# Optimization experiments

Hardware: AMD Instinct MI355X
Metric: run time of the kernel (lower is better)

## Reference

```python
import jax, jax.numpy as jnp
import numpy as np

B, S, D = 8, 4096, 1024  # batch, seq, input_dim == hidden_dim


def setup_inputs() -> dict:
    key = jax.random.key(0)
    k1, k2, k3, k4, k5 = jax.random.split(key, 5)
    s = 1.0 / np.sqrt(D)
    return {
        "q": jax.random.normal(k1, (B, S, D), dtype=jnp.float32),
        "k": jax.random.normal(k2, (B, D), dtype=jnp.float32),
        # torch Linear(in,out,bias=False) weight is [out,in]; store transposed [in,out]
        "W1": jax.random.uniform(k3, (D, D), dtype=jnp.float32, minval=-s, maxval=s),
        "W2": jax.random.uniform(k4, (D, D), dtype=jnp.float32, minval=-s, maxval=s),
        "V": jax.random.uniform(k5, (D, D), dtype=jnp.float32, minval=-s, maxval=s),
    }


def reference(q, k, W1, W2, V):
    # q: [B,S,D], k: [B,D]
    h_q = jnp.einsum("bsd,dh->bsh", q, W1)          # W1(q): [B,S,H]
    h_k = jnp.einsum("bd,dh->bh", k, W2)[:, None]   # W2(k).unsqueeze(1): [B,1,H]
    scores = jnp.einsum("bsh,hv->bsv", jnp.tanh(h_q + h_k), V)  # [B,S,H]
    weights = jax.nn.softmax(scores, axis=-1)       # softmax over feature dim (as in source)
    values = jnp.sum(weights * q, axis=1)           # [B,D]
    return values, weights
```

## Files before the change

### kernel.cpp

```cpp
#include <hip/hip_runtime.h>
#include <hip/hip_bf16.h>

#define DDIM 1024
#define BATCH 8
#define SEQ 4096
#define MROWS (BATCH*SEQ)

typedef __attribute__((ext_vector_type(8))) short short8;
typedef __attribute__((ext_vector_type(4))) float floatx4;

__device__ inline short f2bf(float f) {
    unsigned int u = __builtin_bit_cast(unsigned int, f);
    unsigned int r = (u + 0x7fffu + ((u >> 16) & 1u)) >> 16;
    return (short)r;
}

__device__ inline float fast_tanh(float x) {
    float e = __expf(2.f * x);
    return 1.f - 2.f / (e + 1.f);
}

typedef const __attribute__((address_space(1))) unsigned int* gas_ptr;
typedef __attribute__((address_space(3))) unsigned int* las_ptr;
__device__ __forceinline__ void gl16(const short* g, short* l) {
    __builtin_amdgcn_global_load_lds((gas_ptr)g, (las_ptr)l, 16, 0, 0);
}

#define VMCNT4 asm volatile("s_waitcnt vmcnt(4)" ::: "memory")
#define VMCNT0 asm volatile("s_waitcnt vmcnt(0)" ::: "memory")
#define BARRIER do { __builtin_amdgcn_sched_barrier(0); __builtin_amdgcn_s_barrier(); \
                     __builtin_amdgcn_sched_barrier(0); } while (0)

__global__ __launch_bounds__(256) void convert_q_kernel(const float* __restrict__ q,
                                                        short* __restrict__ qb) {
    size_t t = (size_t)blockIdx.x * 256 + threadIdx.x;
    const size_t stride = (size_t)2048 * 256;
    for (int it = 0; it < 8; ++it, t += stride) {
        size_t i = t * 8;
        float4 f0 = *(const float4*)(q + i);
        float4 f1 = *(const float4*)(q + i + 4);
        short8 v;
        v[0]=f2bf(f0.x); v[1]=f2bf(f0.y); v[2]=f2bf(f0.z); v[3]=f2bf(f0.w);
        v[4]=f2bf(f1.x); v[5]=f2bf(f1.y); v[6]=f2bf(f1.z); v[7]=f2bf(f1.w);
        *(short8*)(qb + i) = v;
    }
}

__global__ __launch_bounds__(256) void hk_kernel(const float* __restrict__ k,
                                                 const float* __restrict__ W2,
                                                 float* __restrict__ hk) {
    int b  = blockIdx.x >> 4;
    int h0 = (blockIdx.x & 15) * 64;
    int hl = threadIdx.x & 63;
    int dc = threadIdx.x >> 6;
    const float* kb = k + (size_t)b * DDIM;
    float sum = 0.f;
    for (int d = dc * 256; d < dc * 256 + 256; ++d)
        sum += kb[d] * W2[(size_t)d * DDIM + h0 + hl];
    __shared__ float red[4][64];
    red[dc][hl] = sum;
    __syncthreads();
    if (dc == 0)
        hk[(size_t)b * DDIM + h0 + hl] = red[0][hl] + red[1][hl] + red[2][hl] + red[3][hl];
}

__global__ __launch_bounds__(256) void transpose_bf16_kernel(const float* __restrict__ src,
                                                             short* __restrict__ dst) {
    __shared__ float t[32][33];
    int bx = blockIdx.x & 31;
    int by = blockIdx.x >> 5;
    int c  = threadIdx.x & 31;
    int r0 = threadIdx.x >> 5;
    for (int p = 0; p < 4; ++p) {
        int r = p * 8 + r0;
        t[r][c] = src[(size_t)(by * 32 + r) * DDIM + bx * 32 + c];
    }
    __syncthreads();
    for (int p = 0; p < 4; ++p) {
        int r = p * 8 + r0;
        dst[(size_t)(bx * 32 + r) * DDIM + by * 32 + c] = f2bf(t[c][r]);
    }
}

template<int EPI>
__global__ __launch_bounds__(512, 2) void gemm256_kernel(const short* __restrict__ A,
                                                         const short* __restrict__ Bt,
                                                         const float* __restrict__ hk,
                                                         void* __restrict__ Out) {
    __shared__ __align__(16) short lds[2 * 32768];
    int bid = blockIdx.x;
    int swz = (bid & 7) * 64 + (bid >> 3);
    int mt = swz >> 2, nt = swz & 3;
    int m0 = mt * 256, n0 = nt * 256;
    int tid = threadIdx.x, lane = tid & 63, wid = tid >> 6;
    int wm = (wid >> 2) * 16;
    int wn = (wid & 3) * 16;
    int lr = lane & 15, kb = lane >> 4;
    floatx4 acc[8][4] = {};

    int srow = lane >> 3;
    int sblk = (lane & 7) ^ srow;
    const size_t arow_base = (size_t)(m0 + wid * 8 + srow) * DDIM + sblk * 8;
    const size_t brow_base = (size_t)(n0 + wid * 8 + srow) * DDIM + sblk * 8;
    const int lds_st = wid * 512 + lane * 8;

    auto stage = [&](int buf, int isB, int h, int t) {
        const short* src = isB ? Bt : A;
        size_t rb = isB ? brow_base : arow_base;
        #pragma unroll
        for (int r = 0; r < 2; ++r)
            gl16(src + rb + (size_t)(h * 128 + r * 64) * DDIM + t * 64,
                 lds + buf * 32768 + isB * 16384 + h * 8192 + r * 4096 + lds_st);
    };
    auto rdA = [&](int buf, int mi, int kk) -> short8 {
        int row = wm + mi * 32 + lr;
        return *(const short8*)(lds + buf * 32768 + (row >> 7) * 8192 +
                                (row & 127) * 64 + (((kk * 4 + kb) ^ (row & 7)) * 8));
    };
    auto rdB = [&](int buf, int ni, int kk) -> short8 {
        int row = wn + ni * 64 + lr;
        return *(const short8*)(lds + buf * 32768 + 16384 + (row >> 7) * 8192 +
                                (row & 127) * 64 + (((kk * 4 + kb) ^ (row & 7)) * 8));
    };

    stage(0, 0, 0, 0); stage(0, 1, 0, 0); stage(0, 1, 1, 0); stage(0, 0, 1, 0);
    VMCNT4;
    BARRIER;

    short8 a0[4][2], a1[4][2], b0[2][2], b1[2][2];

    for (int t = 0; t < 15; ++t) {
        int cb = t & 1, nb = cb ^ 1;
        stage(nb, 0, 0, t + 1);
        #pragma unroll
        for (int mi = 0; mi < 4; ++mi)
            #pragma unroll
            for (int kk = 0; kk < 2; ++kk) a0[mi][kk] = rdA(cb, mi, kk);
        #pragma unroll
        for (int ni = 0; ni < 2; ++ni)
            #pragma unroll
            for (int kk = 0; kk < 2; ++kk) b0[ni][kk] = rdB(cb, ni, kk);
        __builtin_amdgcn_s_setprio(1);
        #pragma unroll
        for (int mi = 0; mi < 4; ++mi)
            #pragma unroll
            for (int ni = 0; ni < 2; ++ni)
                #pragma unroll
                for (int kk = 0; kk < 2; ++kk)
                    acc[mi][ni] = __builtin_amdgcn_mfma_f32_16x16x32_bf16(a0[mi][kk], b0[ni][kk], acc[mi][ni], 0, 0, 0);
        __builtin_amdgcn_s_setprio(0);
        VMCNT4;
        BARRIER;
        stage(nb, 1, 0, t + 1);
        #pragma unroll
        for (int ni = 0; ni < 2; ++ni)
            #pragma unroll
            for (int kk = 0; kk < 2; ++kk) b1[ni][kk] = rdB(cb, ni + 2, kk);
        __builtin_amdgcn_s_setprio(1);
        #pragma unroll
        for (int mi = 0; mi < 4; ++mi)
            #pragma unroll
            for (int ni = 0; ni < 2; ++ni)
                #pragma unroll
                for (int kk = 0; kk < 2; ++kk)
                    acc[mi][ni + 2] = __builtin_amdgcn_mfma_f32_16x16x32_bf16(a0[mi][kk], b1[ni][kk], acc[mi][ni + 2], 0, 0, 0);
        __builtin_amdgcn_s_setprio(0);
        VMCNT4;
        BARRIER;
        stage(nb, 1, 1, t + 1);
        #pragma unroll
        for (int mi = 0; mi < 4; ++mi)
            #pragma unroll
            for (int kk = 0; kk < 2; ++kk) a1[mi][kk] = rdA(cb, mi + 4, kk);
        __builtin_amdgcn_s_setprio(1);
        #pragma unroll
        for (int mi = 0; mi < 4; ++mi)
            #pragma unroll
            for (int ni = 0; ni < 2; ++ni)
                #pragma unroll
                for (int kk = 0; kk < 2; ++kk)
                    acc[mi + 4][ni] = __builtin_amdgcn_mfma_f32_16x16x32_bf16(a1[mi][kk], b0[ni][kk], acc[mi + 4][ni], 0, 0, 0);
        __builtin_amdgcn_s_setprio(0);
        BARRIER;
        stage(nb, 0, 1, t + 1);
        __builtin_amdgcn_s_setprio(1);
        #pragma unroll
        for (int mi = 0; mi < 4; ++mi)
            #pragma unroll
            for (int ni = 0; ni < 2; ++ni)
                #pragma unroll
                for (int kk = 0; kk < 2; ++kk)
                    acc[mi + 4][ni + 2] = __builtin_amdgcn_mfma_f32_16x16x32_bf16(a1[mi][kk], b1[ni][kk], acc[mi + 4][ni + 2], 0, 0, 0);
        __builtin_amdgcn_s_setprio(0);
        VMCNT4;
        BARRIER;
    }

    {
        const int cb = 1;
        #pragma unroll
        for (int mi = 0; mi < 4; ++mi)
            #pragma unroll
            for (int kk = 0; kk < 2; ++kk) a0[mi][kk] = rdA(cb, mi, kk);
        #pragma unroll
        for (int ni = 0; ni < 2; ++ni)
            #pragma unroll
            for (int kk = 0; kk < 2; ++kk) b0[ni][kk] = rdB(cb, ni, kk);
        #pragma unroll
        for (int mi = 0; mi < 4; ++mi)
            #pragma unroll
            for (int ni = 0; ni < 2; ++ni)
                #pragma unroll
                for (int kk = 0; kk < 2; ++kk)
                    acc[mi][ni] = __builtin_amdgcn_mfma_f32_16x16x32_bf16(a0[mi][kk], b0[ni][kk], acc[mi][ni], 0, 0, 0);
        VMCNT0;
        BARRIER;
        #pragma unroll
        for (int ni = 0; ni < 2; ++ni)
            #pragma unroll
            for (int kk = 0; kk < 2; ++kk) b1[ni][kk] = rdB(cb, ni + 2, kk);
        #pragma unroll
        for (int mi = 0; mi < 4; ++mi)
            #pragma unroll
            for (int kk = 0; kk < 2; ++kk) a1[mi][kk] = rdA(cb, mi + 4, kk);
        #pragma unroll
        for (int mi = 0; mi < 4; ++mi)
            #pragma unroll
            for (int ni = 0; ni < 2; ++ni)
                #pragma unroll
                for (int kk = 0; kk < 2; ++kk) {
                    acc[mi][ni + 2]     = __builtin_amdgcn_mfma_f32_16x16x32_bf16(a0[mi][kk], b1[ni][kk], acc[mi][ni + 2], 0, 0, 0);
                    acc[mi + 4][ni]     = __builtin_amdgcn_mfma_f32_16x16x32_bf16(a1[mi][kk], b0[ni][kk], acc[mi + 4][ni], 0, 0, 0);
                    acc[mi + 4][ni + 2] = __builtin_amdgcn_mfma_f32_16x16x32_bf16(a1[mi][kk], b1[ni][kk], acc[mi + 4][ni + 2], 0, 0, 0);
                }
    }

    int rr = lane >> 4;
    if constexpr (EPI == 0) {
        short* H = (short*)Out;
        int bidx = m0 >> 12;
        #pragma unroll
        for (int ni = 0; ni < 4; ++ni) {
            int col = n0 + wn + ni * 64 + lr;
            float hkv = hk[(size_t)bidx * DDIM + col];
            #pragma unroll
            for (int mi = 0; mi < 8; ++mi)
                #pragma unroll
                for (int j = 0; j < 4; ++j) {
                    int row = m0 + wm + mi * 32 + rr * 4 + j;
                    H[(size_t)row * DDIM + col] = f2bf(fast_tanh(acc[mi][ni][j] + hkv));
                }
        }
    } else {
        float* S = (float*)Out;
        #pragma unroll
        for (int ni = 0; ni < 4; ++ni) {
            int col = n0 + wn + ni * 64 + lr;
            #pragma unroll
            for (int mi = 0; mi < 8; ++mi)
                #pragma unroll
                for (int j = 0; j < 4; ++j) {
                    int row = m0 + wm + mi * 32 + rr * 4 + j;
                    S[(size_t)row * DDIM + col] = acc[mi][ni][j];
                }
        }
    }
}

__global__ __launch_bounds__(256) void softmax_wsum_kernel(float* __restrict__ weights,
                                                           const float* __restrict__ q,
                                                           float* __restrict__ partials) {
    int blk   = blockIdx.x;
    int b     = blk >> 8;
    int chunk = blk & 255;
    int tid   = threadIdx.x;
    int lane  = tid & 63, wid = tid >> 6;

    float pv[4][4] = {};
    size_t rowbase = ((size_t)b * SEQ + (size_t)chunk * 16 + (size_t)wid * 4) * DDIM;
    #pragma unroll 1
    for (int r = 0; r < 4; ++r) {
        float* wp = weights + rowbase + (size_t)r * DDIM;
        float4 x[4];
        #pragma unroll
        for (int kk = 0; kk < 4; ++kk)
            x[kk] = *(const float4*)(wp + lane * 4 + kk * 256);
        float ls = 0.f;
        #pragma unroll
        for (int kk = 0; kk < 4; ++kk) {
            x[kk].x = __expf(x[kk].x); x[kk].y = __expf(x[kk].y);
            x[kk].z = __expf(x[kk].z); x[kk].w = __expf(x[kk].w);
            ls += x[kk].x + x[kk].y + x[kk].z + x[kk].w;
        }
        #pragma unroll
        for (int o = 32; o > 0; o >>= 1) ls += __shfl_xor(ls, o);
        float inv = 1.f / ls;
        const float* qp = q + rowbase + (size_t)r * DDIM;
        #pragma unroll
        for (int kk = 0; kk < 4; ++kk) {
            float4 w4;
            w4.x = x[kk].x * inv; w4.y = x[kk].y * inv;
            w4.z = x[kk].z * inv; w4.w = x[kk].w * inv;
            *(float4*)(wp + lane * 4 + kk * 256) = w4;
            float4 q4 = *(const float4*)(qp + lane * 4 + kk * 256);
            pv[kk][0] += w4.x * q4.x; pv[kk][1] += w4.y * q4.y;
            pv[kk][2] += w4.z * q4.z; pv[kk][3] += w4.w * q4.w;
        }
    }

    __shared__ float red[4][DDIM];
    #pragma unroll
    for (int kk = 0; kk < 4; ++kk)
        *(float4*)(&red[wid][lane * 4 + kk * 256]) = *(float4*)(&pv[kk][0]);
    __syncthreads();
    #pragma unroll
    for (int kk = 0; kk < 4; ++kk) {
        int d = tid + kk * 256;
        partials[(size_t)blk * DDIM + d] = red[0][d] + red[1][d] + red[2][d] + red[3][d];
    }
}

__global__ __launch_bounds__(256) void reduce_values_kernel(const float* __restrict__ partials,
                                                            float* __restrict__ values) {
    int gid = blockIdx.x * 256 + threadIdx.x;
    int b = gid >> 10, v = gid & 1023;
    float s = 0.f;
    for (int c = 0; c < 256; ++c)
        s += partials[((size_t)b * 256 + c) * DDIM + v];
    values[gid] = s;
}

extern "C" void kernel_launch(void* const* d_in, const int* in_sizes, int n_in,
                              void* d_out, int out_size, void* d_ws, size_t ws_size,
                              hipStream_t stream) {
    const float* q  = (const float*)d_in[0];
    const float* k  = (const float*)d_in[1];
    const float* W1 = (const float*)d_in[2];
    const float* W2 = (const float*)d_in[3];
    const float* V  = (const float*)d_in[4];

    float* values  = (float*)d_out;
    float* weights = (float*)d_out + (size_t)BATCH * DDIM;
    short* q_bf = (short*)weights;

    char* ws = (char*)d_ws;
    float* hk = (float*)ws;         ws += (((size_t)BATCH * DDIM * 4) + 255) & ~(size_t)255;
    short* W1T = (short*)ws;        ws += (size_t)DDIM * DDIM * 2;
    short* VT  = (short*)ws;        ws += (size_t)DDIM * DDIM * 2;
    short* H   = (short*)ws;        ws += (size_t)MROWS * DDIM * 2;
    float* partials = (float*)ws;

    convert_q_kernel<<<dim3(2048), dim3(256), 0, stream>>>(q, q_bf);
    hk_kernel<<<dim3(128), dim3(256), 0, stream>>>(k, W2, hk);
    transpose_bf16_kernel<<<dim3(1024), dim3(256), 0, stream>>>(W1, W1T);
    transpose_bf16_kernel<<<dim3(1024), dim3(256), 0, stream>>>(V, VT);
    gemm256_kernel<0><<<dim3(512), dim3(512), 0, stream>>>(q_bf, W1T, hk, (void*)H);
    gemm256_kernel<1><<<dim3(512), dim3(512), 0, stream>>>(H, VT, nullptr, (void*)weights);
    softmax_wsum_kernel<<<dim3(2048), dim3(256), 0, stream>>>(weights, q, partials);
    reduce_values_kernel<<<dim3(32), dim3(256), 0, stream>>>(partials, values);
}
```

Before: 281.3 us.

## Fuse prep kernels, emit bf16 exp scores, and read them in softmax

Merges the q conversion, the two weight transposes and the hk projection into one prep launch. The second GEMM now writes exp(scores) as bf16 into a workspace buffer instead of fp32 scores into the output. The softmax kernel reads this half-width buffer and only normalises and writes the final weights. H now lives in the unused second half of the weights output region. Together these cut launch count and the fp32 score write/read traffic, at the cost of bf16 rounding of exp values, no max subtraction before exp, and reliance on reusing the output buffer as scratch.

```diff
diff --git a/kernel.cpp b/kernel.cpp
--- a/kernel.cpp
+++ b/kernel.cpp
@@ -14,6 +14,10 @@
     unsigned int r = (u + 0x7fffu + ((u >> 16) & 1u)) >> 16;
     return (short)r;
 }
+__device__ inline float bf2f(short s) {
+    unsigned int u = ((unsigned int)(unsigned short)s) << 16;
+    return __builtin_bit_cast(float, u);
+}
 
 __device__ inline float fast_tanh(float x) {
     float e = __expf(2.f * x);
@@ -31,54 +35,60 @@
 #define BARRIER do { __builtin_amdgcn_sched_barrier(0); __builtin_amdgcn_s_barrier(); \
                      __builtin_amdgcn_sched_barrier(0); } while (0)
 
-__global__ __launch_bounds__(256) void convert_q_kernel(const float* __restrict__ q,
-                                                        short* __restrict__ qb) {
-    size_t t = (size_t)blockIdx.x * 256 + threadIdx.x;
-    const size_t stride = (size_t)2048 * 256;
-    for (int it = 0; it < 8; ++it, t += stride) {
-        size_t i = t * 8;
-        float4 f0 = *(const float4*)(q + i);
-        float4 f1 = *(const float4*)(q + i + 4);
-        short8 v;
-        v[0]=f2bf(f0.x); v[1]=f2bf(f0.y); v[2]=f2bf(f0.z); v[3]=f2bf(f0.w);
-        v[4]=f2bf(f1.x); v[5]=f2bf(f1.y); v[6]=f2bf(f1.z); v[7]=f2bf(f1.w);
-        *(short8*)(qb + i) = v;
-    }
-}
-
-__global__ __launch_bounds__(256) void hk_kernel(const float* __restrict__ k,
-                                                 const float* __restrict__ W2,
-                                                 float* __restrict__ hk) {
-    int b  = blockIdx.x >> 4;
-    int h0 = (blockIdx.x & 15) * 64;
-    int hl = threadIdx.x & 63;
-    int dc = threadIdx.x >> 6;
-    const float* kb = k + (size_t)b * DDIM;
-    float sum = 0.f;
-    for (int d = dc * 256; d < dc * 256 + 256; ++d)
-        sum += kb[d] * W2[(size_t)d * DDIM + h0 + hl];
-    __shared__ float red[4][64];
-    red[dc][hl] = sum;
-    __syncthreads();
-    if (dc == 0)
-        hk[(size_t)b * DDIM + h0 + hl] = red[0][hl] + red[1][hl] + red[2][hl] + red[3][hl];
-}
-
-__global__ __launch_bounds__(256) void transpose_bf16_kernel(const float* __restrict__ src,
-                                                             short* __restrict__ dst) {
-    __shared__ float t[32][33];
-    int bx = blockIdx.x & 31;
-    int by = blockIdx.x >> 5;
-    int c  = threadIdx.x & 31;
-    int r0 = threadIdx.x >> 5;
-    for (int p = 0; p < 4; ++p) {
-        int r = p * 8 + r0;
-        t[r][c] = src[(size_t)(by * 32 + r) * DDIM + bx * 32 + c];
-    }
-    __syncthreads();
-    for (int p = 0; p < 4; ++p) {
-        int r = p * 8 + r0;
-        dst[(size_t)(bx * 32 + r) * DDIM + by * 32 + c] = f2bf(t[c][r]);
+__global__ __launch_bounds__(256) void prep_kernel(const float* __restrict__ q,
+                                                   short* __restrict__ qb,
+                                                   const float* __restrict__ W1,
+                                                   short* __restrict__ W1T,
+                                                   const float* __restrict__ V,
+                                                   short* __restrict__ VT,
+                                                   const float* __restrict__ k,
+                                                   const float* __restrict__ W2,
+                                                   float* __restrict__ hk) {
+    int bid = blockIdx.x;
+    if (bid < 2048) {
+        size_t t = (size_t)bid * 256 + threadIdx.x;
+        const size_t stride = (size_t)2048 * 256;
+        for (int it = 0; it < 8; ++it, t += stride) {
+            size_t i = t * 8;
+            float4 f0 = *(const float4*)(q + i);
+            float4 f1 = *(const float4*)(q + i + 4);
+            short8 v;
+            v[0]=f2bf(f0.x); v[1]=f2bf(f0.y); v[2]=f2bf(f0.z); v[3]=f2bf(f0.w);
+            v[4]=f2bf(f1.x); v[5]=f2bf(f1.y); v[6]=f2bf(f1.z); v[7]=f2bf(f1.w);
+            *(short8*)(qb + i) = v;
+        }
+    } else if (bid < 4096) {
+        const float* src = (bid < 3072) ? W1 : V;
+        short* dst = (bid < 3072) ? W1T : VT;
+        int tb = (bid - 2048) & 1023;
+        __shared__ float t[32][33];
+        int bx = tb & 31, by = tb >> 5;
+        int c  = threadIdx.x & 31;
+        int r0 = threadIdx.x >> 5;
+        for (int p = 0; p < 4; ++p) {
+            int r = p * 8 + r0;
+            t[r][c] = src[(size_t)(by * 32 + r) * DDIM + bx * 32 + c];
+        }
+        __syncthreads();
+        for (int p = 0; p < 4; ++p) {
+            int r = p * 8 + r0;
+            dst[(size_t)(bx * 32 + r) * DDIM + by * 32 + c] = f2bf(t[c][r]);
+        }
+    } else {
+        int hb = bid - 4096;
+        int b  = hb >> 4;
+        int h0 = (hb & 15) * 64;
+        int hl = threadIdx.x & 63;
+        int dc = threadIdx.x >> 6;
+        const float* kb = k + (size_t)b * DDIM;
+        float sum = 0.f;
+        for (int d = dc * 256; d < dc * 256 + 256; ++d)
+            sum += kb[d] * W2[(size_t)d * DDIM + h0 + hl];
+        __shared__ float red[4][64];
+        red[dc][hl] = sum;
+        __syncthreads();
+        if (dc == 0)
+            hk[(size_t)b * DDIM + h0 + hl] = red[0][hl] + red[1][hl] + red[2][hl] + red[3][hl];
     }
 }
 
@@ -86,7 +96,7 @@
 __global__ __launch_bounds__(512, 2) void gemm256_kernel(const short* __restrict__ A,
                                                          const short* __restrict__ Bt,
                                                          const float* __restrict__ hk,
-                                                         void* __restrict__ Out) {
+                                                         short* __restrict__ Out) {
     __shared__ __align__(16) short lds[2 * 32768];
     int bid = blockIdx.x;
     int swz = (bid & 7) * 64 + (bid >> 3);
@@ -237,7 +247,6 @@
 
     int rr = lane >> 4;
     if constexpr (EPI == 0) {
-        short* H = (short*)Out;
         int bidx = m0 >> 12;
         #pragma unroll
         for (int ni = 0; ni < 4; ++ni) {
@@ -248,11 +257,10 @@
                 #pragma unroll
                 for (int j = 0; j < 4; ++j) {
                     int row = m0 + wm + mi * 32 + rr * 4 + j;
-                    H[(size_t)row * DDIM + col] = f2bf(fast_tanh(acc[mi][ni][j] + hkv));
+                    Out[(size_t)row * DDIM + col] = f2bf(fast_tanh(acc[mi][ni][j] + hkv));
                 }
         }
     } else {
-        float* S = (float*)Out;
         #pragma unroll
         for (int ni = 0; ni < 4; ++ni) {
             int col = n0 + wn + ni * 64 + lr;
@@ -261,13 +269,14 @@
                 #pragma unroll
                 for (int j = 0; j < 4; ++j) {
                     int row = m0 + wm + mi * 32 + rr * 4 + j;
-                    S[(size_t)row * DDIM + col] = acc[mi][ni][j];
+                    Out[(size_t)row * DDIM + col] = f2bf(__expf(acc[mi][ni][j]));
                 }
         }
     }
 }
 
-__global__ __launch_bounds__(256) void softmax_wsum_kernel(float* __restrict__ weights,
+__global__ __launch_bounds__(256) void softmax_wsum_kernel(const short* __restrict__ E,
+                                                           float* __restrict__ weights,
                                                            const float* __restrict__ q,
                                                            float* __restrict__ partials) {
     int blk   = blockIdx.x;
@@ -276,47 +285,63 @@
     int tid   = threadIdx.x;
     int lane  = tid & 63, wid = tid >> 6;
 
-    float pv[4][4] = {};
+    float pv[2][8] = {};
     size_t rowbase = ((size_t)b * SEQ + (size_t)chunk * 16 + (size_t)wid * 4) * DDIM;
     #pragma unroll 1
     for (int r = 0; r < 4; ++r) {
-        float* wp = weights + rowbase + (size_t)r * DDIM;
-        float4 x[4];
-        #pragma unroll
-        for (int kk = 0; kk < 4; ++kk)
-            x[kk] = *(const float4*)(wp + lane * 4 + kk * 256);
+        const short* ep = E + rowbase + (size_t)r * DDIM;
+        float x[2][8];
         float ls = 0.f;
         #pragma unroll
-        for (int kk = 0; kk < 4; ++kk) {
-            x[kk].x = __expf(x[kk].x); x[kk].y = __expf(x[kk].y);
-            x[kk].z = __expf(x[kk].z); x[kk].w = __expf(x[kk].w);
-            ls += x[kk].x + x[kk].y + x[kk].z + x[kk].w;
+        for (int kk = 0; kk < 2; ++kk) {
+            short8 v = *(const short8*)(ep + lane * 8 + kk * 512);
+            #pragma unroll
+            for (int j = 0; j < 8; ++j) { x[kk][j] = bf2f(v[j]); ls += x[kk][j]; }
         }
         #pragma unroll
         for (int o = 32; o > 0; o >>= 1) ls += __shfl_xor(ls, o);
         float inv = 1.f / ls;
+        float* wp = weights + rowbase + (size_t)r * DDIM;
         const float* qp = q + rowbase + (size_t)r * DDIM;
         #pragma unroll
-        for (int kk = 0; kk < 4; ++kk) {
-            float4 w4;
-            w4.x = x[kk].x * inv; w4.y = x[kk].y * inv;
-            w4.z = x[kk].z * inv; w4.w = x[kk].w * inv;
-            *(float4*)(wp + lane * 4 + kk * 256) = w4;
-            float4 q4 = *(const float4*)(qp + lane * 4 + kk * 256);
-            pv[kk][0] += w4.x * q4.x; pv[kk][1] += w4.y * q4.y;
-            pv[kk][2] += w4.z * q4.z; pv[kk][3] += w4.w * q4.w;
+        for (int kk = 0; kk < 2; ++kk) {
+            int d = lane * 8 + kk * 512;
+            float4 w4a, w4b;
+            w4a.x = x[kk][0] * inv; w4a.y = x[kk][1] * inv;
+            w4a.z = x[kk][2] * inv; w4a.w = x[kk][3] * inv;
+            w4b.x = x[kk][4] * inv; w4b.y = x[kk][5] * inv;
+            w4b.z = x[kk][6] * inv; w4b.w = x[kk][7] * inv;
+            *(float4*)(wp + d)     = w4a;
+            *(float4*)(wp + d + 4) = w4b;
+            float4 q4a = *(const float4*)(qp + d);
+            float4 q4b = *(const float4*)(qp + d + 4);
+            pv[kk][0] += w4a.x * q4a.x; pv[kk][1] += w4a.y * q4a.y;
+            pv[kk][2] += w4a.z * q4a.z; pv[kk][3] += w4a.w * q4a.w;
+            pv[kk][4] += w4b.x * q4b.x; pv[kk][5] += w4b.y * q4b.y;
+            pv[kk][6] += w4b.z * q4b.z; pv[kk][7] += w4b.w * q4b.w;
         }
     }
 
     __shared__ float red[4][DDIM];
     #pragma unroll
-    for (int kk = 0; kk < 4; ++kk)
-        *(float4*)(&red[wid][lane * 4 + kk * 256]) = *(float4*)(&pv[kk][0]);
+    for (int kk = 0; kk < 2; ++kk) {
+        int d = lane * 8 + kk * 512;
+        *(float4*)(&red[wid][d])     = *(float4*)(&pv[kk][0]);
+        *(float4*)(&red[wid][d + 4]) = *(float4*)(&pv[kk][4]);
+    }
     __syncthreads();
-    #pragma unroll
-    for (int kk = 0; kk < 4; ++kk) {
-        int d = tid + kk * 256;
-        partials[(size_t)blk * DDIM + d] = red[0][d] + red[1][d] + red[2][d] + red[3][d];
+    {
+        int d = tid * 4;
+        float4 s0 = *(float4*)(&red[0][d]);
+        float4 s1 = *(float4*)(&red[1][d]);
+        float4 s2 = *(float4*)(&red[2][d]);
+        float4 s3 = *(float4*)(&red[3][d]);
+        float4 o;
+        o.x = s0.x + s1.x + s2.x + s3.x;
+        o.y = s0.y + s1.y + s2.y + s3.y;
+        o.z = s0.z + s1.z + s2.z + s3.z;
+        o.w = s0.w + s1.w + s2.w + s3.w;
+        *(float4*)(partials + (size_t)blk * DDIM + d) = o;
     }
 }
 
@@ -342,20 +367,18 @@
     float* values  = (float*)d_out;
     float* weights = (float*)d_out + (size_t)BATCH * DDIM;
     short* q_bf = (short*)weights;
+    short* H    = q_bf + (size_t)MROWS * DDIM;
 
     char* ws = (char*)d_ws;
     float* hk = (float*)ws;         ws += (((size_t)BATCH * DDIM * 4) + 255) & ~(size_t)255;
     short* W1T = (short*)ws;        ws += (size_t)DDIM * DDIM * 2;
     short* VT  = (short*)ws;        ws += (size_t)DDIM * DDIM * 2;
-    short* H   = (short*)ws;        ws += (size_t)MROWS * DDIM * 2;
+    short* E   = (short*)ws;        ws += (size_t)MROWS * DDIM * 2;
     float* partials = (float*)ws;
 
-    convert_q_kernel<<<dim3(2048), dim3(256), 0, stream>>>(q, q_bf);
-    hk_kernel<<<dim3(128), dim3(256), 0, stream>>>(k, W2, hk);
-    transpose_bf16_kernel<<<dim3(1024), dim3(256), 0, stream>>>(W1, W1T);
-    transpose_bf16_kernel<<<dim3(1024), dim3(256), 0, stream>>>(V, VT);
-    gemm256_kernel<0><<<dim3(512), dim3(512), 0, stream>>>(q_bf, W1T, hk, (void*)H);
-    gemm256_kernel<1><<<dim3(512), dim3(512), 0, stream>>>(H, VT, nullptr, (void*)weights);
-    softmax_wsum_kernel<<<dim3(2048), dim3(256), 0, stream>>>(weights, q, partials);
+    prep_kernel<<<dim3(4224), dim3(256), 0, stream>>>(q, q_bf, W1, W1T, V, VT, k, W2, hk);
+    gemm256_kernel<0><<<dim3(512), dim3(512), 0, stream>>>(q_bf, W1T, hk, H);
+    gemm256_kernel<1><<<dim3(512), dim3(512), 0, stream>>>(H, VT, nullptr, E);
+    softmax_wsum_kernel<<<dim3(2048), dim3(256), 0, stream>>>(E, weights, q, partials);
     reduce_values_kernel<<<dim3(32), dim3(256), 0, stream>>>(partials, values);
 }
```

After: 278.2 us. About the same (-1.1%).
